# Performance work log

Hardware: AMD Instinct MI355X
Metric: run time of the kernel (lower is better)

Reference implementation:

```python
import jax, jax.numpy as jnp
import numpy as np

FTYPE = ((0, 16), (1, 16), (2, 8))   # [(order, multiplicity)], C = 16*1 + 16*2 + 8*2 = 64
DIM = 64
MAX_ORDER = 2
NUM_BASIS = 2 * MAX_ORDER + 1        # [1, cos a, sin a, cos 2a, sin 2a]
V = 50000
E = 800000
LN_EPS = 1e-5


def _transport(features, transporters, ftype):
    """Apply per-irrep rotation rho_n(g) to each edge's gathered feature. features:(E,C)."""
    blocks = []
    offset = 0
    for order, mult in ftype:
        d = 1 if order == 0 else 2
        C = mult * d
        blk = features[:, offset:offset + C]
        if order == 0:
            blocks.append(blk)
        else:
            b = blk.reshape(-1, mult, 2)                      # (E, mult, 2)
            phi = order * transporters
            c, s = jnp.cos(phi), jnp.sin(phi)
            R = jnp.stack([jnp.stack([c, -s], -1),
                           jnp.stack([s,  c], -1)], -2)        # (E, 2, 2)
            rot = jnp.einsum('emd,erd->emr', b, R)             # rotate each 2-vector
            blocks.append(rot.reshape(-1, C))
        offset += C
    return jnp.concatenate(blocks, axis=1)


def _angle_basis(angles):
    """Circular harmonic basis for the equivariant kernel: (E, NUM_BASIS)."""
    cols = [jnp.ones_like(angles)]
    for k in range(1, MAX_ORDER + 1):
        cols.append(jnp.cos(k * angles))
        cols.append(jnp.sin(k * angles))
    return jnp.stack(cols, axis=1)


def _regular_nonlin(x, ftype):
    """ReLU on scalar (rho_0) channels; norm-gated softplus on vector channels."""
    blocks = []
    offset = 0
    for order, mult in ftype:
        d = 1 if order == 0 else 2
        C = mult * d
        blk = x[:, offset:offset + C]
        if order == 0:
            blocks.append(jax.nn.relu(blk))
        else:
            b = blk.reshape(-1, mult, 2)
            norms = jnp.clip(jnp.linalg.norm(b, axis=-1, keepdims=True), 1e-8, None)
            out_b = b * (jax.nn.softplus(norms) / norms)
            blocks.append(out_b.reshape(-1, C))
        offset += C
    return jnp.concatenate(blocks, axis=1)


def _gem_block(x, edge_index, angles, transporters, K_self, W_neigh, ln_gamma, ln_beta):
    src, tgt = edge_index[0], edge_index[1]
    # self-interaction
    out = x @ K_self.T                                        # (V, C_out)
    # gather + parallel transport
    f_q = _transport(x[src], transporters, FTYPE)             # (E, C_in)
    # per-edge equivariant kernel applied via fused einsum:
    #   K_neigh[e] = sum_b basis[e,b] * W_neigh[b]  ;  msg[e] = K_neigh[e] @ f_q[e]
    basis = _angle_basis(angles)                              # (E, B)
    tmp = jnp.einsum('boi,ei->ebo', W_neigh, f_q)             # (E, B, C_out)
    msg = jnp.einsum('eb,ebo->eo', basis, tmp)                # (E, C_out)
    # scatter-add messages into targets
    out = out + jax.ops.segment_sum(msg, tgt, num_segments=V)
    # LayerNorm
    mu = jnp.mean(out, axis=-1, keepdims=True)
    var = jnp.var(out, axis=-1, keepdims=True)
    h = (out - mu) * jax.lax.rsqrt(var + LN_EPS) * ln_gamma + ln_beta
    # regular nonlinearity + identity residual (dim_in == dim_out)
    h = _regular_nonlin(h, FTYPE)
    return h + x


def setup_inputs() -> dict:
    key = jax.random.key(0)
    ks = jax.random.split(key, 8)
    x = jax.random.normal(ks[0], (V, DIM), jnp.float32)
    edge_index = jax.random.randint(ks[1], (2, E), 0, V)
    angles = jax.random.uniform(ks[2], (E,), jnp.float32, 0.0, 2.0 * np.pi)
    transporters = jax.random.uniform(ks[3], (E,), jnp.float32, 0.0, 2.0 * np.pi)
    K_self = jax.random.normal(ks[4], (DIM, DIM), jnp.float32) / np.sqrt(DIM)
    W_neigh = jax.random.normal(ks[5], (NUM_BASIS, DIM, DIM), jnp.float32) / np.sqrt(DIM * NUM_BASIS)
    ln_gamma = jnp.ones((DIM,), jnp.float32)
    ln_beta = jnp.zeros((DIM,), jnp.float32)
    return {"x": x, "edge_index": edge_index, "angles": angles, "transporters": transporters,
            "K_self": K_self, "W_neigh": W_neigh, "ln_gamma": ln_gamma, "ln_beta": ln_beta}


def reference(x, edge_index, angles, transporters, K_self, W_neigh, ln_gamma, ln_beta):
    return _gem_block(x, edge_index, angles, transporters, K_self, W_neigh, ln_gamma, ln_beta)
```

## Files before the change

kernel.cpp:

```cpp
#include <hip/hip_runtime.h>

#define VN 50000
#define EN 800000
#define CAP 48
#define USH 392

typedef short short8 __attribute__((ext_vector_type(8)));
typedef float float4v __attribute__((ext_vector_type(4)));

#define WS_GBF   0
#define WS_WHI   128
#define WS_WLO   12416
#define WS_POS   24704
#define WS_REC   74704
#define WS_A_BYTES ((size_t)(74704 + 50000 * 48 * 4) * 4)

__device__ __forceinline__ float bf2f(unsigned short u) {
    return __uint_as_float(((unsigned int)u) << 16);
}
__device__ __forceinline__ unsigned short f2bf(float f) {
    unsigned int x = __float_as_uint(f);
    return (unsigned short)((x + 0x7fffu + ((x >> 16) & 1u)) >> 16);
}
__device__ __forceinline__ float ldf(const void* p, int isbf, size_t i) {
    return isbf ? bf2f(((const unsigned short*)p)[i]) : ((const float*)p)[i];
}

__device__ __forceinline__ int block_detect(const void* xv) {
    __shared__ int flg;
    if (threadIdx.x < 64) {
        unsigned short w = ((const unsigned short*)xv)[2 * threadIdx.x];
        int e = (w >> 7) & 0xFF;
        bool ok = (e >= 0x70 && e <= 0x85) || (w == 0);
        unsigned long long m = __ballot(ok);
        if (threadIdx.x == 0) flg = (__popcll(m) >= 40) ? 1 : 0;
    }
    __syncthreads();
    return flg;
}

__device__ __forceinline__ void convert_dev(int idx, const void* Ks,
                                            const void* Wn, const void* gma,
                                            const void* bta, float* ws, int isbf) {
    if (idx < 128) {
        const void* p = (idx < 64) ? gma : bta;
        ws[WS_GBF + idx] = ldf(p, isbf, idx & 63);
    } else {
        int m2 = idx - 128;
        int j = m2 & 7;
        int chunk = m2 >> 3;
        int slot = chunk >> 6;
        int ln = chunk & 63;
        int ks = slot >> 2, wv = slot & 3;
        int k = ks * 32 + ((ln >> 4) * 8) + j;
        int n = wv * 16 + (ln & 15);
        float wvl;
        if (k < 320) {
            int b = k >> 6, i = k & 63;
            wvl = ldf(Wn, isbf, (b * 64 + n) * 64 + i);
        } else {
            wvl = ldf(Ks, isbf, n * 64 + (k - 320));
        }
        unsigned short hi = f2bf(wvl);
        unsigned short lo = f2bf(wvl - bf2f(hi));
        ((unsigned short*)(ws + WS_WHI))[m2] = hi;
        ((unsigned short*)(ws + WS_WLO))[m2] = lo;
    }
}

template <bool PAY>
__global__ __launch_bounds__(512) void conv_place(
    const void* xv, const int* __restrict__ eidx, const void* angv,
    const void* trpv, const void* Ks, const void* Wn, const void* gma,
    const void* bta, float* __restrict__ ws) {
    const int isbf = block_detect(xv);
    int gtid = blockIdx.x * 512 + threadIdx.x;
    if (gtid < 128 + 24576) convert_dev(gtid, Ks, Wn, gma, bta, ws, isbf);
    if (gtid < EN) {
        int tgt = eidx[EN + gtid];
        int slot = atomicAdd(&((int*)(ws + WS_POS))[tgt], 1);
        if (slot < CAP) {
            if (PAY) {
                uint4 r;
                r.x = (unsigned int)eidx[gtid];
                r.y = __float_as_uint(ldf(angv, isbf, gtid));
                r.z = __float_as_uint(ldf(trpv, isbf, gtid));
                r.w = 0u;
                ((uint4*)(ws + WS_REC))[(size_t)tgt * CAP + slot] = r;
            } else {
                ((int*)(ws + WS_REC))[(size_t)tgt * CAP + slot] = gtid;
            }
        }
    }
}

template <bool BF, bool PAY>
__device__ __forceinline__ void gem_body(
    const void* xv, const int* __restrict__ eidx, const void* angv,
    const void* trpv, const float* __restrict__ ws, void* __restrict__ outv,
    float* Ledge, unsigned short* Uhi, unsigned short* Ulo, int* degs) {
    const int t = threadIdx.x;
    const int lane = t & 63;
    const int w = t >> 6;
    const int v0 = blockIdx.x * 16;
    const int* pos = (const int*)(ws + WS_POS);
    float* Cst = Ledge;

    if (t < 16) degs[t] = min(pos[v0 + t], CAP);
    __syncthreads();

    if (t < 16 * CAP) {
        int n = t / CAP, s = t - n * CAP;
        if (s < degs[n]) {
            unsigned int srcb;
            float aphi, tphi;
            if (PAY) {
                uint4 r = ((const uint4*)(ws + WS_REC))[(size_t)(v0 + n) * CAP + s];
                srcb = r.x;
                aphi = __uint_as_float(r.y);
                tphi = __uint_as_float(r.z);
            } else {
                int e = ((const int*)(ws + WS_REC))[(size_t)(v0 + n) * CAP + s];
                srcb = (unsigned int)eidx[e];
                aphi = BF ? bf2f(((const unsigned short*)angv)[e])
                          : ((const float*)angv)[e];
                tphi = BF ? bf2f(((const unsigned short*)trpv)[e])
                          : ((const float*)trpv)[e];
            }
            float st, ct, sa, ca;
            __sincosf(tphi, &st, &ct);
            __sincosf(aphi, &sa, &ca);
            float4v pa = {__uint_as_float(srcb), ct, st, ca};
            float4v pb = {sa, fmaf(ca, ca, -sa * sa), 2.f * ca * sa, 0.f};
            *(float4v*)&Ledge[t * 8] = pa;
            *(float4v*)&Ledge[t * 8 + 4] = pb;
        }
    }
    __syncthreads();

    const int v = v0 + w;
    const int d = degs[w];
    const bool isv = lane >= 16, o2 = lane >= 48;
    const float sgn = (lane & 1) ? 1.f : -1.f;
    float a0 = 0.f, a1 = 0.f, a2 = 0.f, a3 = 0.f, a4 = 0.f;

    auto edge1 = [&](float4v pa, float4v pb, float xg) {
        float ct = pa[1], st = pa[2];
        float c2t = fmaf(ct, ct, -st * st);
        float s2t = 2.f * ct * st;
        float cl = isv ? (o2 ? c2t : ct) : 1.f;
        float sl = isv ? (o2 ? s2t : st) : 0.f;
        float prt = __shfl_xor(xg, 1, 64);
        float fq = fmaf(cl, xg, sgn * sl * prt);
        a0 += fq;
        a1 = fmaf(pa[3], fq, a1);
        a2 = fmaf(pb[0], fq, a2);
        a3 = fmaf(pb[1], fq, a3);
        a4 = fmaf(pb[2], fq, a4);
    };
    auto loadx = [&](unsigned int s) -> float {
        if (BF) return bf2f(((const unsigned short*)xv)[(size_t)s * 64 + lane]);
        else    return ((const float*)xv)[(size_t)s * 64 + lane];
    };

    const float* Lb = &Ledge[w * CAP * 8];
    int j = 0;
    for (; j + 4 <= d; j += 4) {
        float4v pa0 = *(const float4v*)&Lb[(j + 0) * 8];
        float4v pb0 = *(const float4v*)&Lb[(j + 0) * 8 + 4];
        float4v pa1 = *(const float4v*)&Lb[(j + 1) * 8];
        float4v pb1 = *(const float4v*)&Lb[(j + 1) * 8 + 4];
        float4v pa2 = *(const float4v*)&Lb[(j + 2) * 8];
        float4v pb2 = *(const float4v*)&Lb[(j + 2) * 8 + 4];
        float4v pa3 = *(const float4v*)&Lb[(j + 3) * 8];
        float4v pb3 = *(const float4v*)&Lb[(j + 3) * 8 + 4];
        float x0 = loadx(__float_as_uint(pa0[0]));
        float x1 = loadx(__float_as_uint(pa1[0]));
        float x2 = loadx(__float_as_uint(pa2[0]));
        float x3 = loadx(__float_as_uint(pa3[0]));
        edge1(pa0, pb0, x0); edge1(pa1, pb1, x1);
        edge1(pa2, pb2, x2); edge1(pa3, pb3, x3);
    }
    for (; j < d; ++j) {
        float4v pa = *(const float4v*)&Lb[j * 8];
        float4v pb = *(const float4v*)&Lb[j * 8 + 4];
        edge1(pa, pb, loadx(__float_as_uint(pa[0])));
    }

    float xown = BF ? bf2f(((const unsigned short*)xv)[(size_t)v * 64 + lane])
                    : ((const float*)xv)[(size_t)v * 64 + lane];

    auto wrU = [&](int c, float val) {
        unsigned short h = f2bf(val);
        unsigned short l = f2bf(val - bf2f(h));
        Uhi[w * USH + c * 64 + lane] = h;
        Ulo[w * USH + c * 64 + lane] = l;
    };
    wrU(0, a0); wrU(1, a1); wrU(2, a2); wrU(3, a3); wrU(4, a4); wrU(5, xown);
    __syncthreads();

    const int mcol = lane & 15, q = lane >> 4;
    if (w < 4) {
        const unsigned short* Whi = (const unsigned short*)(ws + WS_WHI);
        const unsigned short* Wlo = (const unsigned short*)(ws + WS_WLO);
        float4v acc = (float4v){0.f, 0.f, 0.f, 0.f};
#pragma unroll
        for (int ks = 0; ks < 12; ++ks) {
            short8 ahi = *(const short8*)&Uhi[mcol * USH + ks * 32 + q * 8];
            short8 alo = *(const short8*)&Ulo[mcol * USH + ks * 32 + q * 8];
            short8 bhi = *(const short8*)(Whi + ((size_t)(ks * 4 + w) * 64 + lane) * 8);
            short8 blo = *(const short8*)(Wlo + ((size_t)(ks * 4 + w) * 64 + lane) * 8);
            acc = __builtin_amdgcn_mfma_f32_16x16x32_bf16(ahi, bhi, acc, 0, 0, 0);
            acc = __builtin_amdgcn_mfma_f32_16x16x32_bf16(alo, bhi, acc, 0, 0, 0);
            acc = __builtin_amdgcn_mfma_f32_16x16x32_bf16(ahi, blo, acc, 0, 0, 0);
        }
#pragma unroll
        for (int reg = 0; reg < 4; ++reg)
            Cst[(q * 4 + reg) * 68 + w * 16 + mcol] = acc[reg];
    }
    __syncthreads();

    const float* gbf = ws + WS_GBF;
    float s = Cst[w * 68 + lane];
    float s1 = s, s2v = s * s;
#pragma unroll
    for (int off = 32; off > 0; off >>= 1) {
        s1 += __shfl_xor(s1, off, 64);
        s2v += __shfl_xor(s2v, off, 64);
    }
    float mu = s1 * (1.f / 64.f);
    float var = s2v * (1.f / 64.f) - mu * mu;
    float h = (s - mu) * rsqrtf(var + 1e-5f) * gbf[lane] + gbf[64 + lane];

    float prt = __shfl_xor(h, 1, 64);
    float rlt;
    if (lane < 16) {
        rlt = fmaxf(h, 0.f);
    } else {
        float nrm = sqrtf(h * h + prt * prt);
        nrm = fmaxf(nrm, 1e-8f);
        float sp = (nrm > 20.f) ? nrm : log1pf(__expf(nrm));
        rlt = h * (sp / nrm);
    }
    float xr = bf2f(Uhi[w * USH + 320 + lane]) + bf2f(Ulo[w * USH + 320 + lane]);
    float res = rlt + xr;
    if (BF) ((unsigned short*)outv)[(size_t)v * 64 + lane] = f2bf(res);
    else    ((float*)outv)[(size_t)v * 64 + lane] = res;
}

template <bool PAY>
__global__ __launch_bounds__(1024, 2) void gem_kernel(
    const void* xv, const int* __restrict__ eidx, const void* angv,
    const void* trpv, const float* __restrict__ ws, void* __restrict__ outv) {
    __shared__ float Ledge[16 * CAP * 8];
    __shared__ unsigned short Uhi[16 * USH];
    __shared__ unsigned short Ulo[16 * USH];
    __shared__ int degs[16];

    const int isbf = block_detect(xv);
    if (isbf) gem_body<true, PAY>(xv, eidx, angv, trpv, ws, outv,
                                  Ledge, Uhi, Ulo, degs);
    else      gem_body<false, PAY>(xv, eidx, angv, trpv, ws, outv,
                                   Ledge, Uhi, Ulo, degs);
}

extern "C" void kernel_launch(void* const* d_in, const int* in_sizes, int n_in,
                              void* d_out, int out_size, void* d_ws, size_t ws_size,
                              hipStream_t stream) {
    const void* x   = d_in[0];
    const int* eidx = (const int*)d_in[1];
    const void* ang = d_in[2];
    const void* trp = d_in[3];
    const void* Ks  = d_in[4];
    const void* Wn  = d_in[5];
    const void* gma = d_in[6];
    const void* bta = d_in[7];
    float* ws = (float*)d_ws;

    hipMemsetAsync(ws + WS_POS, 0, VN * sizeof(int), stream);
    if (ws_size >= WS_A_BYTES) {
        conv_place<true><<<1563, 512, 0, stream>>>(x, eidx, ang, trp, Ks, Wn,
                                                   gma, bta, ws);
        gem_kernel<true><<<VN / 16, 1024, 0, stream>>>(x, eidx, ang, trp, ws,
                                                       d_out);
    } else {
        conv_place<false><<<1563, 512, 0, stream>>>(x, eidx, ang, trp, Ks, Wn,
                                                    gma, bta, ws);
        gem_kernel<false><<<VN / 16, 1024, 0, stream>>>(x, eidx, ang, trp, ws,
                                                        d_out);
    }
}
```

Before: 198.8 us.

## Halve gem block to 8 vertices, precompute per-group edge coefficients, prefetch gathers

The gem kernel now handles 8 vertices per 512-thread block instead of 16 per 1024, so more blocks can be resident and per-block barriers are cheaper. The MFMA A-operand rows are folded onto the 8 valid rows. Per-edge shared-memory records grow to 16 floats and hold precomputed cos/sin of twice the angle, plus a per-lane-group rotation slot. This removes per-edge selects and double-angle math in the inner loop and replaces the sign multiply with an XOR. The edge loop also software-prefetches the next four gathered x rows. The cost is twice as much LDS per edge, and half the MFMA rows now do redundant work.

```diff
diff --git a/kernel.cpp b/kernel.cpp
--- a/kernel.cpp
+++ b/kernel.cpp
@@ -98,20 +98,18 @@
 __device__ __forceinline__ void gem_body(
     const void* xv, const int* __restrict__ eidx, const void* angv,
     const void* trpv, const float* __restrict__ ws, void* __restrict__ outv,
-    float* Ledge, unsigned short* Uhi, unsigned short* Ulo, int* degs) {
+    float* Ledge, unsigned short* Uhi, unsigned short* Ulo) {
     const int t = threadIdx.x;
     const int lane = t & 63;
     const int w = t >> 6;
-    const int v0 = blockIdx.x * 16;
+    const int v0 = blockIdx.x * 8;
     const int* pos = (const int*)(ws + WS_POS);
     float* Cst = Ledge;
 
-    if (t < 16) degs[t] = min(pos[v0 + t], CAP);
-    __syncthreads();
-
-    if (t < 16 * CAP) {
+    if (t < 8 * CAP) {
         int n = t / CAP, s = t - n * CAP;
-        if (s < degs[n]) {
+        int dn = min(pos[v0 + n], CAP);
+        if (s < dn) {
             unsigned int srcb;
             float aphi, tphi;
             if (PAY) {
@@ -130,66 +128,71 @@
             float st, ct, sa, ca;
             __sincosf(tphi, &st, &ct);
             __sincosf(aphi, &sa, &ca);
-            float4v pa = {__uint_as_float(srcb), ct, st, ca};
-            float4v pb = {sa, fmaf(ca, ca, -sa * sa), 2.f * ca * sa, 0.f};
-            *(float4v*)&Ledge[t * 8] = pa;
-            *(float4v*)&Ledge[t * 8 + 4] = pb;
+            float c2a = fmaf(ca, ca, -sa * sa), s2a = 2.f * ca * sa;
+            float c2t = fmaf(ct, ct, -st * st), s2t = 2.f * ct * st;
+            float* L = &Ledge[t * 16];
+            *(float4v*)(L)      = (float4v){__uint_as_float(srcb), ca, sa, c2a};
+            *(float4v*)(L + 4)  = (float4v){1.f, 0.f, s2a, 0.f};
+            *(float4v*)(L + 8)  = (float4v){ct, st, s2a, 0.f};
+            *(float4v*)(L + 12) = (float4v){c2t, s2t, s2a, 0.f};
         }
     }
     __syncthreads();
 
     const int v = v0 + w;
-    const int d = degs[w];
-    const bool isv = lane >= 16, o2 = lane >= 48;
-    const float sgn = (lane & 1) ? 1.f : -1.f;
+    const int d = min(pos[v], CAP);
+    const int g = (lane < 16) ? 0 : ((lane < 48) ? 1 : 2);
+    const int grpoff = 4 + 4 * g;
+    const unsigned int smask = (lane & 1) ? 0u : 0x80000000u;
     float a0 = 0.f, a1 = 0.f, a2 = 0.f, a3 = 0.f, a4 = 0.f;
 
-    auto edge1 = [&](float4v pa, float4v pb, float xg) {
-        float ct = pa[1], st = pa[2];
-        float c2t = fmaf(ct, ct, -st * st);
-        float s2t = 2.f * ct * st;
-        float cl = isv ? (o2 ? c2t : ct) : 1.f;
-        float sl = isv ? (o2 ? s2t : st) : 0.f;
-        float prt = __shfl_xor(xg, 1, 64);
-        float fq = fmaf(cl, xg, sgn * sl * prt);
-        a0 += fq;
-        a1 = fmaf(pa[3], fq, a1);
-        a2 = fmaf(pb[0], fq, a2);
-        a3 = fmaf(pb[1], fq, a3);
-        a4 = fmaf(pb[2], fq, a4);
-    };
+    const float* Lb = &Ledge[w * CAP * 16];
     auto loadx = [&](unsigned int s) -> float {
         if (BF) return bf2f(((const unsigned short*)xv)[(size_t)s * 64 + lane]);
         else    return ((const float*)xv)[(size_t)s * 64 + lane];
     };
-
-    const float* Lb = &Ledge[w * CAP * 8];
-    int j = 0;
-    for (; j + 4 <= d; j += 4) {
-        float4v pa0 = *(const float4v*)&Lb[(j + 0) * 8];
-        float4v pb0 = *(const float4v*)&Lb[(j + 0) * 8 + 4];
-        float4v pa1 = *(const float4v*)&Lb[(j + 1) * 8];
-        float4v pb1 = *(const float4v*)&Lb[(j + 1) * 8 + 4];
-        float4v pa2 = *(const float4v*)&Lb[(j + 2) * 8];
-        float4v pb2 = *(const float4v*)&Lb[(j + 2) * 8 + 4];
-        float4v pa3 = *(const float4v*)&Lb[(j + 3) * 8];
-        float4v pb3 = *(const float4v*)&Lb[(j + 3) * 8 + 4];
-        float x0 = loadx(__float_as_uint(pa0[0]));
-        float x1 = loadx(__float_as_uint(pa1[0]));
-        float x2 = loadx(__float_as_uint(pa2[0]));
-        float x3 = loadx(__float_as_uint(pa3[0]));
-        edge1(pa0, pb0, x0); edge1(pa1, pb1, x1);
-        edge1(pa2, pb2, x2); edge1(pa3, pb3, x3);
-    }
-    for (; j < d; ++j) {
-        float4v pa = *(const float4v*)&Lb[j * 8];
-        float4v pb = *(const float4v*)&Lb[j * 8 + 4];
-        edge1(pa, pb, loadx(__float_as_uint(pa[0])));
-    }
+    auto edge1 = [&](int j, float xg) {
+        const float* L = &Lb[j * 16];
+        float4v sh = *(const float4v*)L;
+        float4v gr = *(const float4v*)(L + grpoff);
+        float prt = __shfl_xor(xg, 1, 64);
+        float tmp = __uint_as_float(__float_as_uint(gr[1] * prt) ^ smask);
+        float fq = fmaf(gr[0], xg, tmp);
+        a0 += fq;
+        a1 = fmaf(sh[1], fq, a1);
+        a2 = fmaf(sh[2], fq, a2);
+        a3 = fmaf(sh[3], fq, a3);
+        a4 = fmaf(gr[2], fq, a4);
+    };
+
+    const int nb = d >> 2;
+    float y0, y1, y2, y3;
+    if (nb > 0) {
+        y0 = loadx(__float_as_uint(Lb[0 * 16]));
+        y1 = loadx(__float_as_uint(Lb[1 * 16]));
+        y2 = loadx(__float_as_uint(Lb[2 * 16]));
+        y3 = loadx(__float_as_uint(Lb[3 * 16]));
+    }
+    for (int b = 0; b < nb; ++b) {
+        float z0, z1, z2, z3;
+        const bool more = (b + 1 < nb);
+        if (more) {
+            int j4 = (b + 1) * 4;
+            z0 = loadx(__float_as_uint(Lb[(j4 + 0) * 16]));
+            z1 = loadx(__float_as_uint(Lb[(j4 + 1) * 16]));
+            z2 = loadx(__float_as_uint(Lb[(j4 + 2) * 16]));
+            z3 = loadx(__float_as_uint(Lb[(j4 + 3) * 16]));
+        }
+        int j0 = b * 4;
+        edge1(j0 + 0, y0); edge1(j0 + 1, y1);
+        edge1(j0 + 2, y2); edge1(j0 + 3, y3);
+        if (more) { y0 = z0; y1 = z1; y2 = z2; y3 = z3; }
+    }
+    for (int j = nb * 4; j < d; ++j)
+        edge1(j, loadx(__float_as_uint(Lb[j * 16])));
 
     float xown = BF ? bf2f(((const unsigned short*)xv)[(size_t)v * 64 + lane])
                     : ((const float*)xv)[(size_t)v * 64 + lane];
-
     auto wrU = [&](int c, float val) {
         unsigned short h = f2bf(val);
         unsigned short l = f2bf(val - bf2f(h));
@@ -201,13 +204,14 @@
 
     const int mcol = lane & 15, q = lane >> 4;
     if (w < 4) {
+        const int mrow = mcol & 7;
         const unsigned short* Whi = (const unsigned short*)(ws + WS_WHI);
         const unsigned short* Wlo = (const unsigned short*)(ws + WS_WLO);
         float4v acc = (float4v){0.f, 0.f, 0.f, 0.f};
 #pragma unroll
         for (int ks = 0; ks < 12; ++ks) {
-            short8 ahi = *(const short8*)&Uhi[mcol * USH + ks * 32 + q * 8];
-            short8 alo = *(const short8*)&Ulo[mcol * USH + ks * 32 + q * 8];
+            short8 ahi = *(const short8*)&Uhi[mrow * USH + ks * 32 + q * 8];
+            short8 alo = *(const short8*)&Ulo[mrow * USH + ks * 32 + q * 8];
             short8 bhi = *(const short8*)(Whi + ((size_t)(ks * 4 + w) * 64 + lane) * 8);
             short8 blo = *(const short8*)(Wlo + ((size_t)(ks * 4 + w) * 64 + lane) * 8);
             acc = __builtin_amdgcn_mfma_f32_16x16x32_bf16(ahi, bhi, acc, 0, 0, 0);
@@ -249,19 +253,16 @@
 }
 
 template <bool PAY>
-__global__ __launch_bounds__(1024, 2) void gem_kernel(
+__global__ __launch_bounds__(512, 8) void gem_kernel(
     const void* xv, const int* __restrict__ eidx, const void* angv,
     const void* trpv, const float* __restrict__ ws, void* __restrict__ outv) {
-    __shared__ float Ledge[16 * CAP * 8];
-    __shared__ unsigned short Uhi[16 * USH];
-    __shared__ unsigned short Ulo[16 * USH];
-    __shared__ int degs[16];
+    __shared__ float Ledge[8 * CAP * 16];
+    __shared__ unsigned short Uhi[8 * USH];
+    __shared__ unsigned short Ulo[8 * USH];
 
     const int isbf = block_detect(xv);
-    if (isbf) gem_body<true, PAY>(xv, eidx, angv, trpv, ws, outv,
-                                  Ledge, Uhi, Ulo, degs);
-    else      gem_body<false, PAY>(xv, eidx, angv, trpv, ws, outv,
-                                   Ledge, Uhi, Ulo, degs);
+    if (isbf) gem_body<true, PAY>(xv, eidx, angv, trpv, ws, outv, Ledge, Uhi, Ulo);
+    else      gem_body<false, PAY>(xv, eidx, angv, trpv, ws, outv, Ledge, Uhi, Ulo);
 }
 
 extern "C" void kernel_launch(void* const* d_in, const int* in_sizes, int n_in,
@@ -281,12 +282,12 @@
     if (ws_size >= WS_A_BYTES) {
         conv_place<true><<<1563, 512, 0, stream>>>(x, eidx, ang, trp, Ks, Wn,
                                                    gma, bta, ws);
-        gem_kernel<true><<<VN / 16, 1024, 0, stream>>>(x, eidx, ang, trp, ws,
-                                                       d_out);
+        gem_kernel<true><<<VN / 8, 512, 0, stream>>>(x, eidx, ang, trp, ws,
+                                                     d_out);
     } else {
         conv_place<false><<<1563, 512, 0, stream>>>(x, eidx, ang, trp, Ks, Wn,
                                                     gma, bta, ws);
-        gem_kernel<false><<<VN / 16, 1024, 0, stream>>>(x, eidx, ang, trp, ws,
-                                                        d_out);
-    }
-}
+        gem_kernel<false><<<VN / 8, 512, 0, stream>>>(x, eidx, ang, trp, ws,
+                                                      d_out);
+    }
+}
```

Measured after the change: 199.8 us. Within noise of the previous version (+0.5%).
